# Kernel tuning notes

Hardware: AMD Instinct MI355X
Metric: run time of the kernel (lower is better)

Reference implementation:

```python
import jax, jax.numpy as jnp
import numpy as np
from jax import lax

KS = [3, 5, 7, 9]
DS = [1, 2, 3, 4]
BN_EPS = 1e-5


def setup_inputs() -> dict:
    key = jax.random.key(0)
    ks = jax.random.split(key, 16)
    B, Cin, H, W = 16, 64, 256, 256
    Ce = 64  # out_channels // 2
    inp = {"x": jax.random.normal(ks[0], (B, Cin, H, W), jnp.float32)}
    for i, (k, _) in enumerate(zip(KS, DS)):
        fan_in = Cin * k * k
        inp[f"w{i}"] = jax.random.normal(ks[1 + i], (Ce, Cin, k, k), jnp.float32) / np.sqrt(fan_in)
        inp[f"b{i}"] = jnp.zeros((Ce,), jnp.float32)
    inp["bn_scale"] = jnp.ones((4, Ce), jnp.float32)
    inp["bn_bias"] = jnp.zeros((4, Ce), jnp.float32)
    inp["bn_mean"] = jax.random.normal(ks[5], (4, Ce), jnp.float32) * 0.1
    inp["bn_var"] = jax.random.uniform(ks[6], (4, Ce), jnp.float32, 0.5, 1.5)
    inp["gate_w"] = jax.random.normal(ks[7], (4, Cin), jnp.float32) / np.sqrt(Cin)
    inp["gate_b"] = jnp.zeros((4,), jnp.float32)
    return inp


def _expert(x, w, b, scale, bias, mean, var, k, d):
    pad = d * (k - 1) // 2
    y = lax.conv_general_dilated(
        x, w, window_strides=(2, 2), padding=[(pad, pad), (pad, pad)],
        rhs_dilation=(d, d), dimension_numbers=("NCHW", "OIHW", "NCHW"))
    y = y + b[None, :, None, None]
    inv = scale * lax.rsqrt(var + BN_EPS)
    y = y * inv[None, :, None, None] + (bias - mean * inv)[None, :, None, None]
    return jax.nn.gelu(y, approximate=False)


def reference(x, w0, b0, w1, b1, w2, b2, w3, b3,
              bn_scale, bn_bias, bn_mean, bn_var, gate_w, gate_b):
    B = x.shape[0]
    # Gate: global average pool -> linear -> softmax -> top-2 renormalized
    pooled = x.mean(axis=(2, 3))                    # (B, Cin)
    gates = jax.nn.softmax(pooled @ gate_w.T + gate_b, axis=1)  # (B, 4)
    top2_w, top2_idx = lax.top_k(gates, 2)
    top2_w = top2_w / (top2_w.sum(axis=1, keepdims=True) + 1e-8)
    # Dense compute of all 4 experts (faithful to original module)
    ws, bs = [w0, w1, w2, w3], [b0, b1, b2, b3]
    outs = [
        _expert(x, ws[i], bs[i], bn_scale[i], bn_bias[i], bn_mean[i], bn_var[i], KS[i], DS[i])
        for i in range(4)
    ]
    E = jnp.stack(outs, axis=1)                     # (B, 4, Ce, H/2, W/2)
    sel = jnp.take_along_axis(E, top2_idx[:, :, None, None, None], axis=1)  # (B,2,Ce,h,w)
    weighted = sel * top2_w[:, :, None, None, None]
    # concat top-2 along channel dim == reshape (B,2,Ce,h,w) -> (B,2*Ce,h,w)
    Bc, two, Ce, h, w = weighted.shape
    return weighted.reshape(Bc, two * Ce, h, w)
```

## Files before the change

### kernel.cpp

```cpp
#include <hip/hip_runtime.h>
#include <hip/hip_bf16.h>
#include <math.h>

#define CIN 64
#define CE  64
#define HH  256
#define WW  256
#define OHW 128
#define PW  288
#define PH  288
#define WOFF 19600

typedef __attribute__((ext_vector_type(8))) short bf16x8;
typedef __attribute__((ext_vector_type(4))) float f32x4;

static __device__ __forceinline__ unsigned short f2bf(float f) {
    __hip_bfloat16 h = __float2bfloat16(f);
    return *reinterpret_cast<unsigned short*>(&h);
}

#define GLOAD16(gsrc, ldst)                                                        \
    __builtin_amdgcn_global_load_lds(                                              \
        (const __attribute__((address_space(1))) void*)(gsrc),                     \
        (__attribute__((address_space(3))) void*)(ldst), 16, 0, 0)

template <bool PRE>
__global__ __launch_bounds__(256)
void poolcvt_kernel(const float* __restrict__ x, unsigned short* __restrict__ xbf,
                    float* __restrict__ partial) {
    int blk = blockIdx.x;
    int rc = blockIdx.y;
    int tid = threadIdx.x, lane = tid & 63, wv = tid >> 6;
    int c0 = lane * 4;
    const float* xb = x + (size_t)blk * 8 * (HH * WW);
    unsigned short* pl = xbf + (size_t)blk * (PW * PH) * 8;
    float s[8];
#pragma unroll
    for (int j = 0; j < 8; ++j) s[j] = 0.f;
#pragma unroll 1
    for (int rr = wv; rr < 32; rr += 4) {
        int h = rc * 32 + rr;
        float4 v[8];
#pragma unroll
        for (int j = 0; j < 8; ++j)
            v[j] = *reinterpret_cast<const float4*>(xb + (size_t)j * (HH * WW) + h * WW + c0);
#pragma unroll
        for (int j = 0; j < 8; ++j) s[j] += (v[j].x + v[j].y) + (v[j].z + v[j].w);
        if (PRE) {
            size_t o16 = ((size_t)(16 + h) * PW + 16 + c0);
            unsigned short u[4][8];
#pragma unroll
            for (int j = 0; j < 8; ++j) {
                u[0][j] = f2bf(v[j].x);
                u[1][j] = f2bf(v[j].y);
                u[2][j] = f2bf(v[j].z);
                u[3][j] = f2bf(v[j].w);
            }
#pragma unroll
            for (int cc = 0; cc < 4; ++cc)
                *reinterpret_cast<bf16x8*>(pl + (o16 + cc) * 8) =
                    *reinterpret_cast<const bf16x8*>(u[cc]);
        }
    }
    if (PRE) {
        bf16x8 z = (bf16x8)(short)0;
#pragma unroll 1
        for (int i = tid; i < 32 * 32; i += 256) {
            int rr = i >> 5, cc = i & 31;
            int pr = 16 + rc * 32 + rr;
            int pc = (cc < 16) ? cc : (256 + cc);
            *reinterpret_cast<bf16x8*>(pl + ((size_t)pr * PW + pc) * 8) = z;
        }
        if (rc == 0) {
#pragma unroll 1
            for (int i = tid; i < 16 * PW; i += 256)
                *reinterpret_cast<bf16x8*>(pl + (size_t)i * 8) = z;
        }
        if (rc == 7) {
#pragma unroll 1
            for (int i = tid; i < 16 * PW; i += 256)
                *reinterpret_cast<bf16x8*>(pl + ((size_t)(272 * PW) + i) * 8) = z;
        }
    }
#pragma unroll
    for (int j = 0; j < 8; ++j) {
#pragma unroll
        for (int m = 32; m >= 1; m >>= 1) s[j] += __shfl_xor(s[j], m, 64);
    }
    __shared__ float red[4][8];
    if (lane == 0) {
#pragma unroll
        for (int j = 0; j < 8; ++j) red[wv][j] = s[j];
    }
    __syncthreads();
    if (tid < 8) {
        int j = tid;
        float t = (red[0][j] + red[1][j]) + (red[2][j] + red[3][j]);
        partial[(blk * 8 + rc) * 8 + j] = t;
    }
}

__global__ __launch_bounds__(64)
void gate_kernel(const float* __restrict__ partial, const float* __restrict__ gw,
                 const float* __restrict__ gb, int* __restrict__ sel_idx,
                 float* __restrict__ sel_w) {
    int b = blockIdx.x;
    int c = threadIdx.x;
    float p = 0.f;
#pragma unroll
    for (int rc = 0; rc < 8; ++rc)
        p += partial[(((b * 8 + (c >> 3)) * 8) + rc) * 8 + (c & 7)];
    p *= (1.0f / (HH * WW));
    float l[4];
#pragma unroll
    for (int e = 0; e < 4; ++e) l[e] = p * gw[e * CIN + c];
#pragma unroll
    for (int m = 32; m >= 1; m >>= 1) {
#pragma unroll
        for (int e = 0; e < 4; ++e) l[e] += __shfl_xor(l[e], m, 64);
    }
    if (c == 0) {
        float g[4], s = 0.f;
#pragma unroll
        for (int e = 0; e < 4; ++e) l[e] += gb[e];
        float mx = fmaxf(fmaxf(l[0], l[1]), fmaxf(l[2], l[3]));
#pragma unroll
        for (int e = 0; e < 4; ++e) { g[e] = expf(l[e] - mx); s += g[e]; }
#pragma unroll
        for (int e = 0; e < 4; ++e) g[e] /= s;
        int i1 = 0;
        for (int e = 1; e < 4; ++e) if (g[e] > g[i1]) i1 = e;
        int i2 = -1;
        for (int e = 0; e < 4; ++e) {
            if (e == i1) continue;
            if (i2 < 0 || g[e] > g[i2]) i2 = e;
        }
        float den = g[i1] + g[i2] + 1e-8f;
        sel_idx[b * 2 + 0] = i1;
        sel_idx[b * 2 + 1] = i2;
        sel_w[b * 2 + 0] = g[i1] / den;
        sel_w[b * 2 + 1] = g[i2] / den;
    }
}

__global__ void order_kernel(const int* __restrict__ sel_idx, int* __restrict__ ord) {
    if (threadIdx.x == 0) {
        int pos = 0;
        const int pri[4] = {3, 2, 1, 0};
        for (int pi = 0; pi < 4; ++pi)
            for (int bs = 0; bs < 32; ++bs)
                if (sel_idx[bs] == pri[pi]) ord[pos++] = bs;
    }
}

__global__ __launch_bounds__(256)
void wprep_all_kernel(const float* __restrict__ w0, const float* __restrict__ w1,
                      const float* __restrict__ w2, const float* __restrict__ w3,
                      unsigned short* __restrict__ wq) {
    int cb = blockIdx.x;
    int y = blockIdx.y;
    const float* w;
    int g0, k, GE;
    size_t base;
    if (y < 3)       { w = w0; g0 = y;      k = 3; GE = 3;  base = 0; }
    else if (y < 10) { w = w1; g0 = y - 3;  k = 5; GE = 7;  base = 49152; }
    else if (y < 23) { w = w2; g0 = y - 10; k = 7; GE = 13; base = 163840; }
    else             { w = w3; g0 = y - 23; k = 9; GE = 21; base = 376832; }
    int k2 = k * k;
    int t = threadIdx.x, tl = t >> 6, co = t & 63;
    int tap = g0 * 4 + tl;
    unsigned short vals[8];
#pragma unroll
    for (int j = 0; j < 8; ++j) {
        float v = 0.f;
        if (tap < k2) v = w[(size_t)(co * CIN + cb * 8 + j) * k2 + tap];
        vals[j] = f2bf(v);
    }
    *reinterpret_cast<bf16x8*>(&wq[base + (size_t)(cb * GE + g0) * 2048 + t * 8]) =
        *reinterpret_cast<const bf16x8*>(vals);
}

template <int K, int D, int GE, bool EVEN, bool PRE>
__device__ __forceinline__ void conv_body(const float* __restrict__ xb,
                                          const unsigned short* __restrict__ xpb,
                                          const unsigned short* __restrict__ wq,
                                          unsigned short* __restrict__ lds,
                                          f32x4 acc[4][4],
                                          int ih0, int iw0, int lane, int wv, int tid) {
    constexpr int K2 = K * K;
    constexpr int TS = 31 + (K - 1) * D;
    constexpr int S = (TS + 1) / 2;
    constexpr int HPW = S * 8;
    constexpr int PITCH = 2 * HPW;
    constexpr int NRC = (TS + 1) / 2;
    constexpr int NEL = EVEN ? NRC * NRC : TS * 2 * S;
    constexpr int DH = EVEN ? D / 2 : 0;
    constexpr int NPH = 8 * GE;
    int p = lane & 15, hi = lane >> 4;

    if constexpr (PRE) {
        GLOAD16(wq + tid * 8, &lds[WOFF + tid * 8]);
        const unsigned short* wrun = wq + 2048;
        int ph = 1;
        int par = 0;

#pragma unroll 1
        for (int cb = 0; cb < 8; ++cb) {
            asm volatile("s_waitcnt vmcnt(0)" ::: "memory");
            __builtin_amdgcn_s_barrier();
            const unsigned short* xp = xpb + (size_t)cb * (PW * PH) * 8;
#pragma unroll 1
            for (int idx = tid; idx < NEL; idx += 256) {
                int ih, iw;
                if constexpr (EVEN) {
                    int r = idx / NRC, c = idx - r * NRC;
                    ih = ih0 + 16 + 2 * r;
                    iw = iw0 + 16 + 2 * c;
                } else {
                    int r = idx / (2 * S), rem = idx - r * (2 * S);
                    int half = rem >= S ? 1 : 0;
                    int sl = rem - half * S;
                    int c = 2 * sl + half;
                    if (c > TS - 1) c = TS - 1;
                    ih = ih0 + 16 + r;
                    iw = iw0 + 16 + c;
                }
                GLOAD16(xp + ((size_t)ih * PW + iw) * 8, &lds[idx * 8]);
            }
            int kh = hi / K, kw = hi % K;
#pragma unroll 2
            for (int g = 0; g < GE; ++g) {
                asm volatile("s_waitcnt vmcnt(0)" ::: "memory");
                __builtin_amdgcn_s_barrier();
                if (ph < NPH) {
                    GLOAD16(wrun + tid * 8, &lds[WOFF + (par ^ 1) * 2048 + tid * 8]);
                    wrun += 2048;
                    ++ph;
                }
                const unsigned short* wl = &lds[WOFF + par * 2048 + hi * 512 + p * 8];
                bf16x8 a0 = *reinterpret_cast<const bf16x8*>(wl);
                bf16x8 a1 = *reinterpret_cast<const bf16x8*>(wl + 128);
                bf16x8 a2 = *reinterpret_cast<const bf16x8*>(wl + 256);
                bf16x8 a3 = *reinterpret_cast<const bf16x8*>(wl + 384);
                int khc = min(kh, K - 1);
                if constexpr (EVEN) {
                    int ec = p + DH * kw;
                    int erb = wv * 4 + DH * khc;
#pragma unroll
                    for (int j = 0; j < 4; ++j) {
                        const bf16x8 bf = *reinterpret_cast<const bf16x8*>(
                            &lds[((erb + j) * NRC + ec) * 8]);
                        acc[j][0] = __builtin_amdgcn_mfma_f32_16x16x32_bf16(a0, bf, acc[j][0], 0, 0, 0);
                        acc[j][1] = __builtin_amdgcn_mfma_f32_16x16x32_bf16(a1, bf, acc[j][1], 0, 0, 0);
                        acc[j][2] = __builtin_amdgcn_mfma_f32_16x16x32_bf16(a2, bf, acc[j][2], 0, 0, 0);
                        acc[j][3] = __builtin_amdgcn_mfma_f32_16x16x32_bf16(a3, bf, acc[j][3], 0, 0, 0);
                    }
                } else {
                    int ic = 2 * p + D * kw;
                    int bbase = (ic & 1) * HPW + (ic >> 1) * 8;
                    int irb = D * khc + wv * 8;
#pragma unroll
                    for (int j = 0; j < 4; ++j) {
                        const bf16x8 bf = *reinterpret_cast<const bf16x8*>(
                            &lds[(irb + 2 * j) * PITCH + bbase]);
                        acc[j][0] = __builtin_amdgcn_mfma_f32_16x16x32_bf16(a0, bf, acc[j][0], 0, 0, 0);
                        acc[j][1] = __builtin_amdgcn_mfma_f32_16x16x32_bf16(a1, bf, acc[j][1], 0, 0, 0);
                        acc[j][2] = __builtin_amdgcn_mfma_f32_16x16x32_bf16(a2, bf, acc[j][2], 0, 0, 0);
                        acc[j][3] = __builtin_amdgcn_mfma_f32_16x16x32_bf16(a3, bf, acc[j][3], 0, 0, 0);
                    }
                }
                kw += 4;
                if (kw >= K) { kw -= K; ++kh; }
                if (K == 3 && kw >= K) { kw -= K; ++kh; }
                par ^= 1;
            }
        }
    } else {
#pragma unroll 1
        for (int cb = 0; cb < 8; ++cb) {
            __syncthreads();
            const float* xc8 = xb + (size_t)cb * 8 * (HH * WW);
#pragma unroll 1
            for (int idx = tid; idx < NEL; idx += 256) {
                int ih, iw;
                if constexpr (EVEN) {
                    int r = idx / NRC, c = idx - r * NRC;
                    ih = ih0 + 2 * r; iw = iw0 + 2 * c;
                } else {
                    int r = idx / (2 * S), rem = idx - r * (2 * S);
                    int half = rem >= S ? 1 : 0;
                    int sl = rem - half * S;
                    int c = min(2 * sl + half, TS - 1);
                    ih = ih0 + r; iw = iw0 + c;
                }
                int ihc = min(max(ih, 0), HH - 1), iwc = min(max(iw, 0), WW - 1);
                bool ok = ((unsigned)ih < (unsigned)HH) && ((unsigned)iw < (unsigned)WW);
                unsigned short u[8];
                const float* src = xc8 + ihc * WW + iwc;
#pragma unroll
                for (int j = 0; j < 8; ++j) u[j] = f2bf(ok ? src[(size_t)j * (HH * WW)] : 0.f);
                *reinterpret_cast<bf16x8*>(&lds[idx * 8]) = *reinterpret_cast<const bf16x8*>(u);
            }
            __syncthreads();
            const unsigned short* wcb = wq + (size_t)cb * GE * 2048;
#pragma unroll 2
            for (int g = 0; g < GE; ++g) {
                int tap = g * 4 + hi;
                int tapc = tap < K2 ? tap : K2 - 1;
                int kh = tapc / K, kw = tapc % K;
                const unsigned short* wg = wcb + g * 2048 + hi * 512;
                bf16x8 a0 = *reinterpret_cast<const bf16x8*>(wg + p * 8);
                bf16x8 a1 = *reinterpret_cast<const bf16x8*>(wg + 128 + p * 8);
                bf16x8 a2 = *reinterpret_cast<const bf16x8*>(wg + 256 + p * 8);
                bf16x8 a3 = *reinterpret_cast<const bf16x8*>(wg + 384 + p * 8);
                if constexpr (EVEN) {
                    int ec = p + (D / 2) * kw;
                    int erb = wv * 4 + (D / 2) * kh;
#pragma unroll
                    for (int j = 0; j < 4; ++j) {
                        const bf16x8 bf = *reinterpret_cast<const bf16x8*>(
                            &lds[((erb + j) * NRC + ec) * 8]);
                        acc[j][0] = __builtin_amdgcn_mfma_f32_16x16x32_bf16(a0, bf, acc[j][0], 0, 0, 0);
                        acc[j][1] = __builtin_amdgcn_mfma_f32_16x16x32_bf16(a1, bf, acc[j][1], 0, 0, 0);
                        acc[j][2] = __builtin_amdgcn_mfma_f32_16x16x32_bf16(a2, bf, acc[j][2], 0, 0, 0);
                        acc[j][3] = __builtin_amdgcn_mfma_f32_16x16x32_bf16(a3, bf, acc[j][3], 0, 0, 0);
                    }
                } else {
                    int ic = 2 * p + D * kw;
                    int bbase = (ic & 1) * HPW + (ic >> 1) * 8;
                    int irb = D * kh + wv * 8;
#pragma unroll
                    for (int j = 0; j < 4; ++j) {
                        const bf16x8 bf = *reinterpret_cast<const bf16x8*>(
                            &lds[(irb + 2 * j) * PITCH + bbase]);
                        acc[j][0] = __builtin_amdgcn_mfma_f32_16x16x32_bf16(a0, bf, acc[j][0], 0, 0, 0);
                        acc[j][1] = __builtin_amdgcn_mfma_f32_16x16x32_bf16(a1, bf, acc[j][1], 0, 0, 0);
                        acc[j][2] = __builtin_amdgcn_mfma_f32_16x16x32_bf16(a2, bf, acc[j][2], 0, 0, 0);
                        acc[j][3] = __builtin_amdgcn_mfma_f32_16x16x32_bf16(a3, bf, acc[j][3], 0, 0, 0);
                    }
                }
            }
        }
    }
}

template <bool PRE>
__global__ __launch_bounds__(256, 3)
void conv_moe_kernel(const float* __restrict__ x, const unsigned short* __restrict__ xbf,
                     const unsigned short* __restrict__ wq,
                     const float* __restrict__ b0_, const float* __restrict__ b1_,
                     const float* __restrict__ b2_, const float* __restrict__ b3_,
                     const float* __restrict__ bns, const float* __restrict__ bnb,
                     const float* __restrict__ bnm, const float* __restrict__ bnv,
                     const int* __restrict__ sel_idx, const float* __restrict__ sel_w,
                     const int* __restrict__ ord, float* __restrict__ out) {
    __shared__ __align__(16) unsigned short lds[WOFF + 4096];

    int bidx = blockIdx.x;
    int bs = ord[bidx >> 6];
    int tile = bidx & 63;
    int b = bs >> 1, slot = bs & 1;
    int e = sel_idx[bs];
    float gwt = sel_w[bs];
    int oh0 = (tile >> 3) * 16, ow0 = (tile & 7) * 16;
    const float* xb = x + (size_t)b * CIN * HH * WW;
    const unsigned short* xpb = xbf + (size_t)b * 8 * (PW * PH) * 8;
    int tid = threadIdx.x, lane = tid & 63, wv = tid >> 6;
    int p = lane & 15, hi = lane >> 4;

    f32x4 acc[4][4];
#pragma unroll
    for (int j = 0; j < 4; ++j)
#pragma unroll
        for (int ct = 0; ct < 4; ++ct) acc[j][ct] = (f32x4){0.f, 0.f, 0.f, 0.f};

    switch (e) {
        case 0:
            conv_body<3, 1, 3, false, PRE>(xb, xpb, wq, lds, acc, oh0 * 2 - 1, ow0 * 2 - 1, lane, wv, tid);
            break;
        case 1:
            conv_body<5, 2, 7, true, PRE>(xb, xpb, wq + 49152, lds, acc, oh0 * 2 - 4, ow0 * 2 - 4, lane, wv, tid);
            break;
        case 2:
            conv_body<7, 3, 13, false, PRE>(xb, xpb, wq + 163840, lds, acc, oh0 * 2 - 9, ow0 * 2 - 9, lane, wv, tid);
            break;
        default:
            conv_body<9, 4, 21, true, PRE>(xb, xpb, wq + 376832, lds, acc, oh0 * 2 - 16, ow0 * 2 - 16, lane, wv, tid);
            break;
    }

    const float* be = (e == 0) ? b0_ : (e == 1) ? b1_ : (e == 2) ? b2_ : b3_;
    float* ob = out + (size_t)(b * 128 + slot * 64) * (OHW * OHW);
#pragma unroll
    for (int ct = 0; ct < 4; ++ct) {
#pragma unroll
        for (int reg = 0; reg < 4; ++reg) {
            int co = ct * 16 + hi * 4 + reg;
            float bias = be[co];
            float sc = bns[e * CE + co], bi = bnb[e * CE + co];
            float mn = bnm[e * CE + co], vr = bnv[e * CE + co];
            float inv = sc * rsqrtf(vr + 1e-5f);
            float beta = bi - mn * inv + bias * inv;
#pragma unroll
            for (int j = 0; j < 4; ++j) {
                float y = acc[j][ct][reg] * inv + beta;
                float gl = 0.5f * y * (1.0f + erff(y * 0.70710678118654752f));
                int oh = oh0 + wv * 4 + j, ow = ow0 + p;
                ob[(size_t)co * (OHW * OHW) + oh * OHW + ow] = gl * gwt;
            }
        }
    }
}

extern "C" void kernel_launch(void* const* d_in, const int* in_sizes, int n_in,
                              void* d_out, int out_size, void* d_ws, size_t ws_size,
                              hipStream_t stream) {
    const float* x   = (const float*)d_in[0];
    const float* w0  = (const float*)d_in[1];
    const float* b0  = (const float*)d_in[2];
    const float* w1  = (const float*)d_in[3];
    const float* b1  = (const float*)d_in[4];
    const float* w2  = (const float*)d_in[5];
    const float* b2  = (const float*)d_in[6];
    const float* w3  = (const float*)d_in[7];
    const float* b3  = (const float*)d_in[8];
    const float* bns = (const float*)d_in[9];
    const float* bnb = (const float*)d_in[10];
    const float* bnm = (const float*)d_in[11];
    const float* bnv = (const float*)d_in[12];
    const float* gw  = (const float*)d_in[13];
    const float* gb  = (const float*)d_in[14];
    float* out = (float*)d_out;

    char* ws = (char*)d_ws;
    float* partial = (float*)ws;
    int* sel_idx   = (int*)(ws + 32768);
    float* sel_w   = (float*)(ws + 32896);
    int* ord       = (int*)(ws + 33024);
    unsigned short* wq = (unsigned short*)(ws + 33280);
    unsigned short* xbf = (unsigned short*)(ws + 2097152);
    const size_t NEED = 2097152ull + (size_t)128 * PW * PH * 16;
    bool pre = ws_size >= NEED;

    if (pre) poolcvt_kernel<true><<<dim3(128, 8), 256, 0, stream>>>(x, xbf, partial);
    else     poolcvt_kernel<false><<<dim3(128, 8), 256, 0, stream>>>(x, xbf, partial);
    gate_kernel<<<dim3(16), 64, 0, stream>>>(partial, gw, gb, sel_idx, sel_w);
    order_kernel<<<dim3(1), 64, 0, stream>>>(sel_idx, ord);
    wprep_all_kernel<<<dim3(8, 44), 256, 0, stream>>>(w0, w1, w2, w3, wq);

    if (pre)
        conv_moe_kernel<true><<<dim3(2048), 256, 0, stream>>>(
            x, xbf, wq, b0, b1, b2, b3, bns, bnb, bnm, bnv, sel_idx, sel_w, ord, out);
    else
        conv_moe_kernel<false><<<dim3(2048), 256, 0, stream>>>(
            x, xbf, wq, b0, b1, b2, b3, bns, bnb, bnm, bnv, sel_idx, sel_w, ord, out);
}
```

Baseline: 284.7 us.

## Triple-buffer weight slices and precompute input gather offsets per conv tile

The PRE path now computes the per-thread global offsets for the input tile gather once, outside the channel-block loop, instead of recomputing divisions every block. Weight slices are triple-buffered in LDS with a prefetch distance of two. The per-step wait becomes vmcnt(1) rather than a full drain, so the input-tile loads and weight prefetches can overlap MFMA work. This raises LDS use per block by 4 KB, which may lower occupancy, and leans on fragile vmcnt accounting.

```diff
diff --git a/kernel.cpp b/kernel.cpp
--- a/kernel.cpp
+++ b/kernel.cpp
@@ -194,50 +194,57 @@
     constexpr int PITCH = 2 * HPW;
     constexpr int NRC = (TS + 1) / 2;
     constexpr int NEL = EVEN ? NRC * NRC : TS * 2 * S;
+    constexpr int ITER = (NEL + 255) / 256;
     constexpr int DH = EVEN ? D / 2 : 0;
-    constexpr int NPH = 8 * GE;
+    constexpr size_t PLANE = (size_t)PW * PH * 8;
     int p = lane & 15, hi = lane >> 4;
 
     if constexpr (PRE) {
-        GLOAD16(wq + tid * 8, &lds[WOFF + tid * 8]);
-        const unsigned short* wrun = wq + 2048;
-        int ph = 1;
-        int par = 0;
+        int gofs[ITER];
+#pragma unroll
+        for (int i = 0; i < ITER; ++i) {
+            int idx = tid + i * 256;
+            if (idx > NEL - 1) idx = NEL - 1;
+            int ih, iw;
+            if constexpr (EVEN) {
+                int r = idx / NRC, c = idx - r * NRC;
+                ih = ih0 + 16 + 2 * r;
+                iw = iw0 + 16 + 2 * c;
+            } else {
+                int r = idx / (2 * S), rem = idx - r * (2 * S);
+                int half = rem >= S ? 1 : 0;
+                int sl = rem - half * S;
+                int c = 2 * sl + half;
+                if (c > TS - 1) c = TS - 1;
+                ih = ih0 + 16 + r;
+                iw = iw0 + 16 + c;
+            }
+            gofs[i] = (ih * PW + iw) * 8;
+        }
+        int kh0 = hi / K, kw0 = hi % K;
 
 #pragma unroll 1
         for (int cb = 0; cb < 8; ++cb) {
-            asm volatile("s_waitcnt vmcnt(0)" ::: "memory");
             __builtin_amdgcn_s_barrier();
-            const unsigned short* xp = xpb + (size_t)cb * (PW * PH) * 8;
-#pragma unroll 1
-            for (int idx = tid; idx < NEL; idx += 256) {
-                int ih, iw;
-                if constexpr (EVEN) {
-                    int r = idx / NRC, c = idx - r * NRC;
-                    ih = ih0 + 16 + 2 * r;
-                    iw = iw0 + 16 + 2 * c;
-                } else {
-                    int r = idx / (2 * S), rem = idx - r * (2 * S);
-                    int half = rem >= S ? 1 : 0;
-                    int sl = rem - half * S;
-                    int c = 2 * sl + half;
-                    if (c > TS - 1) c = TS - 1;
-                    ih = ih0 + 16 + r;
-                    iw = iw0 + 16 + c;
-                }
-                GLOAD16(xp + ((size_t)ih * PW + iw) * 8, &lds[idx * 8]);
-            }
-            int kh = hi / K, kw = hi % K;
-#pragma unroll 2
+            const unsigned short* xp = xpb + (size_t)cb * PLANE;
+#pragma unroll
+            for (int i = 0; i < ITER; ++i) {
+                if (tid + i * 256 < NEL)
+                    GLOAD16(xp + gofs[i], &lds[(tid + i * 256) * 8]);
+            }
+            const unsigned short* wcb = wq + (size_t)cb * GE * 2048;
+            GLOAD16(wcb + tid * 8, &lds[WOFF + tid * 8]);
+            GLOAD16(wcb + 2048 + tid * 8, &lds[WOFF + 2048 + tid * 8]);
+            int kh = kh0, kw = kw0;
+#pragma unroll 1
             for (int g = 0; g < GE; ++g) {
-                asm volatile("s_waitcnt vmcnt(0)" ::: "memory");
+                if (g == GE - 1) asm volatile("s_waitcnt vmcnt(0)" ::: "memory");
+                else             asm volatile("s_waitcnt vmcnt(1)" ::: "memory");
                 __builtin_amdgcn_s_barrier();
-                if (ph < NPH) {
-                    GLOAD16(wrun + tid * 8, &lds[WOFF + (par ^ 1) * 2048 + tid * 8]);
-                    wrun += 2048;
-                    ++ph;
-                }
-                const unsigned short* wl = &lds[WOFF + par * 2048 + hi * 512 + p * 8];
+                if (g + 2 < GE)
+                    GLOAD16(wcb + (size_t)(g + 2) * 2048 + tid * 8,
+                            &lds[WOFF + ((g + 2) % 3) * 2048 + tid * 8]);
+                const unsigned short* wl = &lds[WOFF + (g % 3) * 2048 + hi * 512 + p * 8];
                 bf16x8 a0 = *reinterpret_cast<const bf16x8*>(wl);
                 bf16x8 a1 = *reinterpret_cast<const bf16x8*>(wl + 128);
                 bf16x8 a2 = *reinterpret_cast<const bf16x8*>(wl + 256);
@@ -272,7 +279,6 @@
                 kw += 4;
                 if (kw >= K) { kw -= K; ++kh; }
                 if (K == 3 && kw >= K) { kw -= K; ++kh; }
-                par ^= 1;
             }
         }
     } else {
@@ -354,7 +360,7 @@
                      const float* __restrict__ bnm, const float* __restrict__ bnv,
                      const int* __restrict__ sel_idx, const float* __restrict__ sel_w,
                      const int* __restrict__ ord, float* __restrict__ out) {
-    __shared__ __align__(16) unsigned short lds[WOFF + 4096];
+    __shared__ __align__(16) unsigned short lds[WOFF + 6144];
 
     int bidx = blockIdx.x;
     int bs = ord[bidx >> 6];
```

Result: no change. 285.7 us (+0.3%).
